# Optimization experiments

Measured on AMD Instinct MI355X. Metric: run time of the kernel, lower is better.

## Reference

```python
import jax, jax.numpy as jnp
import numpy as np

N = 100000   # nodes
E = 600000   # edges
NF = 4       # node feat dim (3 pos + 1 scalar)
EF = 5       # edge feat dim
H = 128      # hidden dim


def setup_inputs() -> dict:
    key = jax.random.key(0)
    ks = jax.random.split(key, 9)

    def lin(k, fan_in, fan_out):
        return (jax.random.normal(k, (fan_in, fan_out), dtype=jnp.float32)
                * (1.0 / np.sqrt(fan_in)))

    x = jax.random.normal(ks[0], (N, NF), dtype=jnp.float32)
    edge_index = jax.random.randint(ks[1], (2, E), 0, N, dtype=jnp.int32)
    edge_attr = jax.random.normal(ks[2], (E, EF), dtype=jnp.float32)

    return {
        "x": x,
        "edge_attr": edge_attr,
        "W1": lin(ks[3], NF, H), "b1": jnp.zeros((H,), jnp.float32),
        "W2": lin(ks[4], H, H),  "b2": jnp.zeros((H,), jnp.float32),
        "Wm1": lin(ks[5], 2 * H + EF, H), "bm1": jnp.zeros((H,), jnp.float32),
        "Wm2": lin(ks[6], H, H),          "bm2": jnp.zeros((H,), jnp.float32),
        "Wm3": lin(ks[7], H, 1),          "bm3": jnp.zeros((1,), jnp.float32),
        "edge_index": edge_index,
    }


def reference(x, edge_attr, W1, b1, W2, b2, Wm1, bm1, Wm2, bm2, Wm3, bm3,
              edge_index):
    src, dst = edge_index[0], edge_index[1]
    n = x.shape[0]

    # GCNConv: add self-loops, symmetric D^{-1/2} A D^{-1/2} normalization.
    loop = jnp.arange(n, dtype=src.dtype)
    src_sl = jnp.concatenate([src, loop])
    dst_sl = jnp.concatenate([dst, loop])
    deg = jax.ops.segment_sum(jnp.ones_like(src_sl, dtype=x.dtype),
                              dst_sl, num_segments=n)
    dinv = jnp.where(deg > 0, jax.lax.rsqrt(deg), 0.0)
    enorm = dinv[src_sl] * dinv[dst_sl]          # [E + N]

    def gcn(h, W, b):
        h = h @ W                                 # transform then propagate
        msg = h[src_sl] * enorm[:, None]          # gather + scale
        return jax.ops.segment_sum(msg, dst_sl, num_segments=n) + b

    h = jax.nn.relu(gcn(x, W1, b1))
    h = gcn(h, W2, b2)

    # Edge classifier: gather endpoints, concat with edge features, MLP.
    edge_emb = jnp.concatenate([h[src], h[dst], edge_attr], axis=1)  # [E, 2H+EF]
    z = jax.nn.relu(edge_emb @ Wm1 + bm1)
    z = jax.nn.relu(z @ Wm2 + bm2)
    out = (z @ Wm3 + bm3)[:, 0]
    return jax.nn.sigmoid(out)
```

## Files before the change

kernel.cpp:

```cpp
#include <hip/hip_runtime.h>
#include <math.h>

#define TPB 256
#define SCAN_T 256
#define SCAN_I 4
#define SCAN_CHUNK 1024

typedef __attribute__((ext_vector_type(8))) short bf16x8;
typedef __attribute__((ext_vector_type(16))) float f32x16;

static __device__ __forceinline__ short f2bf(float a) {
  unsigned ua = __builtin_bit_cast(unsigned, a);
  ua = (ua + 0x7fffu + ((ua >> 16) & 1u)) >> 16;
  return (short)ua;
}
static __device__ __forceinline__ unsigned f2bf_pack(float a, float b) {
  unsigned ua = __builtin_bit_cast(unsigned, a);
  unsigned ub = __builtin_bit_cast(unsigned, b);
  ua = (ua + 0x7fffu + ((ua >> 16) & 1u)) >> 16;
  ub = (ub + 0x7fffu + ((ub >> 16) & 1u)) >> 16;
  return ua | (ub << 16);
}
static __device__ __forceinline__ float bflo(unsigned u) {
  return __builtin_bit_cast(float, u << 16);
}
static __device__ __forceinline__ float bfhi(unsigned u) {
  return __builtin_bit_cast(float, u & 0xffff0000u);
}

__global__ void k_zero_int(int* __restrict__ p, int n) {
  int t = blockIdx.x * TPB + threadIdx.x;
  if (t < n) p[t] = 0;
}

__global__ void k_hist(const int* __restrict__ dst, int* __restrict__ deg, int E) {
  int t = blockIdx.x * TPB + threadIdx.x;
  if (t < E) atomicAdd(&deg[dst[t]], 1);
}

__global__ __launch_bounds__(SCAN_T) void k_scan_local(const int* __restrict__ deg,
                                                       int* __restrict__ loc,
                                                       int* __restrict__ bsum,
                                                       float* __restrict__ dinv, int N) {
  __shared__ int s[SCAN_T];
  int b = blockIdx.x, t = threadIdx.x;
  int base = b * SCAN_CHUNK + t * SCAN_I;
  int v[SCAN_I];
  int sum = 0;
#pragma unroll
  for (int u = 0; u < SCAN_I; u++) {
    int x = (base + u < N) ? deg[base + u] : 0;
    if (base + u < N) dinv[base + u] = rsqrtf((float)x + 1.0f);
    v[u] = sum;
    sum += x;
  }
  s[t] = sum;
  __syncthreads();
#pragma unroll
  for (int off = 1; off < SCAN_T; off <<= 1) {
    int x = (t >= off) ? s[t - off] : 0;
    __syncthreads();
    s[t] += x;
    __syncthreads();
  }
  int excl = (t == 0) ? 0 : s[t - 1];
#pragma unroll
  for (int u = 0; u < SCAN_I; u++)
    if (base + u < N) loc[base + u] = v[u] + excl;
  if (t == SCAN_T - 1) bsum[b] = s[t];
}

__global__ void k_scan_block(int* __restrict__ bsum, int nb) {
  int t = threadIdx.x;
  int i0 = 2 * t, i1 = 2 * t + 1;
  int a = (i0 < nb) ? bsum[i0] : 0;
  int b = (i1 < nb) ? bsum[i1] : 0;
  int s = a + b;
#pragma unroll
  for (int off = 1; off < 64; off <<= 1) {
    int u = __shfl_up(s, off, 64);
    if (t >= off) s += u;
  }
  int excl = s - (a + b);
  if (i0 < nb) bsum[i0] = excl;
  if (i1 < nb) bsum[i1] = excl + a;
}

__global__ void k_scan_add(int* __restrict__ rowoff, const int* __restrict__ bsum,
                           int* __restrict__ cursor, int N) {
  int t = blockIdx.x * TPB + threadIdx.x;
  if (t >= N) return;
  int ro = rowoff[t] + bsum[t / SCAN_CHUNK];
  rowoff[t] = ro;
  cursor[t] = ro;
}

__global__ void k_fill_slots(const int* __restrict__ src, const int* __restrict__ dst,
                             int* __restrict__ cursor, int* __restrict__ slots,
                             int2* __restrict__ epair, int E) {
  int e = blockIdx.x * TPB + threadIdx.x;
  if (e >= E) return;
  int d = dst[e];
  int pos = atomicAdd(&cursor[d], 1);
  slots[pos] = src[e];
  epair[pos] = make_int2(e, d);
}

__global__ void k_gcn1(const float4* __restrict__ x4, const float* __restrict__ W1,
                       const float* __restrict__ dinv, unsigned* __restrict__ tout, int N) {
  int t = blockIdx.x * TPB + threadIdx.x;
  int n = t >> 5;
  if (n >= N) return;
  int q = (t & 31) << 2;
  float4 xv = x4[n];
  float s = dinv[n];
  float r[4];
#pragma unroll
  for (int u = 0; u < 4; u++) {
    int j = q + u;
    r[u] = s * (xv.x * W1[j] + xv.y * W1[128 + j] + xv.z * W1[256 + j] + xv.w * W1[384 + j]);
  }
  uint2 p;
  p.x = f2bf_pack(r[0], r[1]);
  p.y = f2bf_pack(r[2], r[3]);
  *(uint2*)&tout[n * 64 + (q >> 1)] = p;
}

template <bool RELU>
__global__ void k_agg(const unsigned* __restrict__ ts, const int* __restrict__ rowoff,
                      const int* __restrict__ deg, const int* __restrict__ slots,
                      const float* __restrict__ dinv, const float* __restrict__ bias,
                      unsigned* __restrict__ hout, int N) {
  int t = blockIdx.x * TPB + threadIdx.x;
  int n = t >> 4;
  if (n >= N) return;
  int q = (t & 15) << 2;
  uint4 sv = *(const uint4*)&ts[(size_t)n * 64 + q];
  float a0 = bflo(sv.x), a1 = bfhi(sv.x), a2 = bflo(sv.y), a3 = bfhi(sv.y);
  float a4 = bflo(sv.z), a5 = bfhi(sv.z), a6 = bflo(sv.w), a7 = bfhi(sv.w);
  int start = rowoff[n], d = deg[n];
  for (int j0 = 0; j0 < d; j0 += 8) {
    int sl[8];
#pragma unroll
    for (int u = 0; u < 8; u++) {
      int jj = j0 + u;
      sl[u] = (jj < d) ? slots[start + jj] : -1;
    }
    uint4 v[8];
#pragma unroll
    for (int u = 0; u < 8; u++)
      v[u] = (sl[u] >= 0) ? *(const uint4*)&ts[(size_t)sl[u] * 64 + q]
                          : make_uint4(0u, 0u, 0u, 0u);
#pragma unroll
    for (int u = 0; u < 8; u++) {
      a0 += bflo(v[u].x);
      a1 += bfhi(v[u].x);
      a2 += bflo(v[u].y);
      a3 += bfhi(v[u].y);
      a4 += bflo(v[u].z);
      a5 += bfhi(v[u].z);
      a6 += bflo(v[u].w);
      a7 += bfhi(v[u].w);
    }
  }
  float sc = dinv[n];
  int col = q << 1;
  float4 b0 = *(const float4*)&bias[col];
  float4 b1 = *(const float4*)&bias[col + 4];
  a0 = a0 * sc + b0.x;
  a1 = a1 * sc + b0.y;
  a2 = a2 * sc + b0.z;
  a3 = a3 * sc + b0.w;
  a4 = a4 * sc + b1.x;
  a5 = a5 * sc + b1.y;
  a6 = a6 * sc + b1.z;
  a7 = a7 * sc + b1.w;
  if (RELU) {
    a0 = fmaxf(a0, 0.f);
    a1 = fmaxf(a1, 0.f);
    a2 = fmaxf(a2, 0.f);
    a3 = fmaxf(a3, 0.f);
    a4 = fmaxf(a4, 0.f);
    a5 = fmaxf(a5, 0.f);
    a6 = fmaxf(a6, 0.f);
    a7 = fmaxf(a7, 0.f);
  }
  uint4 p;
  p.x = f2bf_pack(a0, a1);
  p.y = f2bf_pack(a2, a3);
  p.z = f2bf_pack(a4, a5);
  p.w = f2bf_pack(a6, a7);
  *(uint4*)&hout[(size_t)n * 64 + q] = p;
}

template <bool BIAS, bool DINV>
__global__ __launch_bounds__(256, 2) void k_gemm_bf(const unsigned* __restrict__ A,
                                                    const float* __restrict__ W,
                                                    const float* __restrict__ bias,
                                                    const float* __restrict__ dinv,
                                                    unsigned* __restrict__ out, int N) {
  __shared__ unsigned sA[64 * 64];
  __shared__ float sDinv[64];
  int tid = threadIdx.x;
  int wv = tid >> 6, lane = tid & 63;
  int rg = wv >> 1, ch = wv & 1;
  int l31 = lane & 31, h = lane >> 5;

  bf16x8 wf[2][8];
  float bcol[2];
#pragma unroll
  for (int t = 0; t < 2; t++) {
    int col = ch * 64 + 2 * l31 + t;
#pragma unroll
    for (int kk = 0; kk < 8; kk++) {
      int kb = kk * 16 + h * 8;
      bf16x8 v;
#pragma unroll
      for (int u = 0; u < 8; u++) v[u] = f2bf(W[(kb + u) * 128 + col]);
      wf[t][kk] = v;
    }
    bcol[t] = BIAS ? bias[col] : 0.f;
  }

  int ntiles = (N + 63) >> 6;
  for (int tile = blockIdx.x; tile < ntiles; tile += gridDim.x) {
    __syncthreads();
    int row0 = tile << 6;
    for (int idx = tid; idx < 1024; idx += 256) {
      int r = idx >> 4, c4 = idx & 15;
      int n = row0 + r;
      uint4 v = (n < N) ? ((const uint4*)A)[(size_t)n * 16 + c4] : make_uint4(0, 0, 0, 0);
      *(uint4*)&sA[r * 64 + ((c4 * 4) ^ ((r & 15) << 2))] = v;
    }
    if (DINV && tid < 64) sDinv[tid] = (row0 + tid < N) ? dinv[row0 + tid] : 0.f;
    __syncthreads();

    int arow = rg * 32 + l31;
    const char* abase = (const char*)sA + arow * 256;
    int swz = (arow & 15) << 4;
    f32x16 acc[2];
#pragma unroll
    for (int t = 0; t < 2; t++) {
#pragma unroll
      for (int r = 0; r < 16; r++) acc[t][r] = 0.f;
    }
#pragma unroll
    for (int kk = 0; kk < 8; kk++) {
      bf16x8 a = *(const bf16x8*)(abase + ((kk * 32 + h * 16) ^ swz));
      acc[0] = __builtin_amdgcn_mfma_f32_32x32x16_bf16(a, wf[0][kk], acc[0], 0, 0, 0);
      acc[1] = __builtin_amdgcn_mfma_f32_32x32x16_bf16(a, wf[1][kk], acc[1], 0, 0, 0);
    }
#pragma unroll
    for (int r = 0; r < 16; r++) {
      int drow = (r & 3) + 8 * (r >> 2) + 4 * h;
      int n = row0 + rg * 32 + drow;
      if (n < N) {
        float v0 = acc[0][r] + bcol[0];
        float v1 = acc[1][r] + bcol[1];
        if (DINV) {
          float s = sDinv[rg * 32 + drow];
          v0 *= s;
          v1 *= s;
        }
        out[(size_t)n * 64 + ch * 32 + l31] = f2bf_pack(v0, v1);
      }
    }
  }
}

__global__ __launch_bounds__(512, 2) void k_gemm_dual(const unsigned* __restrict__ A,
                                                      const float* __restrict__ Wm1,
                                                      const float* __restrict__ bm1,
                                                      unsigned* __restrict__ out_s,
                                                      unsigned* __restrict__ out_d, int N) {
  __shared__ unsigned sA[64 * 64];
  int tid = threadIdx.x;
  int wv = tid >> 6, lane = tid & 63;
  int part = wv >> 2;
  int w4 = wv & 3;
  int rg = w4 >> 1, ch = w4 & 1;
  int l31 = lane & 31, h = lane >> 5;
  const float* W = Wm1 + (size_t)part * 128 * 128;
  unsigned* outp = part ? out_d : out_s;

  bf16x8 wf[2][8];
  float bcol[2];
#pragma unroll
  for (int t = 0; t < 2; t++) {
    int col = ch * 64 + 2 * l31 + t;
#pragma unroll
    for (int kk = 0; kk < 8; kk++) {
      int kb = kk * 16 + h * 8;
      bf16x8 v;
#pragma unroll
      for (int u = 0; u < 8; u++) v[u] = f2bf(W[(kb + u) * 128 + col]);
      wf[t][kk] = v;
    }
    bcol[t] = part ? 0.f : bm1[col];
  }

  int ntiles = (N + 63) >> 6;
  for (int tile = blockIdx.x; tile < ntiles; tile += gridDim.x) {
    __syncthreads();
    int row0 = tile << 6;
    for (int idx = tid; idx < 1024; idx += 512) {
      int r = idx >> 4, c4 = idx & 15;
      int n = row0 + r;
      uint4 v = (n < N) ? ((const uint4*)A)[(size_t)n * 16 + c4] : make_uint4(0, 0, 0, 0);
      *(uint4*)&sA[r * 64 + ((c4 * 4) ^ ((r & 15) << 2))] = v;
    }
    __syncthreads();

    int arow = rg * 32 + l31;
    const char* abase = (const char*)sA + arow * 256;
    int swz = (arow & 15) << 4;
    f32x16 acc[2];
#pragma unroll
    for (int t = 0; t < 2; t++) {
#pragma unroll
      for (int r = 0; r < 16; r++) acc[t][r] = 0.f;
    }
#pragma unroll
    for (int kk = 0; kk < 8; kk++) {
      bf16x8 a = *(const bf16x8*)(abase + ((kk * 32 + h * 16) ^ swz));
      acc[0] = __builtin_amdgcn_mfma_f32_32x32x16_bf16(a, wf[0][kk], acc[0], 0, 0, 0);
      acc[1] = __builtin_amdgcn_mfma_f32_32x32x16_bf16(a, wf[1][kk], acc[1], 0, 0, 0);
    }
#pragma unroll
    for (int r = 0; r < 16; r++) {
      int drow = (r & 3) + 8 * (r >> 2) + 4 * h;
      int n = row0 + rg * 32 + drow;
      if (n < N) {
        float v0 = acc[0][r] + bcol[0];
        float v1 = acc[1][r] + bcol[1];
        outp[(size_t)n * 64 + ch * 32 + l31] = f2bf_pack(v0, v1);
      }
    }
  }
}

__global__ __launch_bounds__(256, 3) void k_edge_mlp(
    const unsigned* __restrict__ a_s, const unsigned* __restrict__ a_d,
    const float* __restrict__ eattr, const int* __restrict__ slots,
    const int2* __restrict__ epair, const float* __restrict__ We,
    const float* __restrict__ Wm2, const float* __restrict__ bm2,
    const float* __restrict__ Wm3, const float* __restrict__ bm3,
    float* __restrict__ out, int E) {
  __shared__ unsigned sZ1[64 * 64];
  __shared__ float sEa[64][5];
  __shared__ int sSrc[64], sDst[64], sEid[64];
  __shared__ float sP[64][2];

  int tid = threadIdx.x;
  int wv = tid >> 6;
  int lane = tid & 63;
  int rg = wv >> 1;
  int ch = wv & 1;
  int l31 = lane & 31;
  int h = lane >> 5;

  bf16x8 bfr[2][8];
#pragma unroll
  for (int t = 0; t < 2; t++) {
    int col = ch * 64 + t * 32 + l31;
#pragma unroll
    for (int kk = 0; kk < 8; kk++) {
      int kb = kk * 16 + h * 8;
      bf16x8 v;
#pragma unroll
      for (int u = 0; u < 8; u++) v[u] = f2bf(Wm2[(kb + u) * 128 + col]);
      bfr[t][kk] = v;
    }
  }
  float wm3c[2], bm2c[2];
#pragma unroll
  for (int t = 0; t < 2; t++) {
    int col = ch * 64 + t * 32 + l31;
    wm3c[t] = Wm3[col];
    bm2c[t] = bm2[col];
  }
  float bm3v = bm3[0];
  float2 we[5];
#pragma unroll
  for (int j = 0; j < 5; j++) we[j] = *(const float2*)(We + j * 128 + 2 * lane);

  int ntiles = (E + 63) >> 6;
  for (int tile = blockIdx.x; tile < ntiles; tile += gridDim.x) {
    __syncthreads();
    int p0 = tile << 6;
    if (tid < 64) {
      int p = p0 + tid;
      int2 ed = (p < E) ? epair[p] : make_int2(0, 0);
      sSrc[tid] = (p < E) ? slots[p] : 0;
      sDst[tid] = ed.y;
      sEid[tid] = ed.x;
    }
    for (int idx = tid; idx < 320; idx += 256) {
      int r = idx / 5, j = idx - r * 5;
      int p = p0 + r;
      int e = (p < E) ? epair[p].x : 0;
      sEa[r][j] = (p < E) ? eattr[(size_t)e * 5 + j] : 0.f;
    }
    __syncthreads();

    unsigned ua[16], ud[16];
#pragma unroll
    for (int i = 0; i < 16; i++) {
      int r = wv * 16 + i;
      ua[i] = a_s[(size_t)sSrc[r] * 64 + lane];
      ud[i] = a_d[(size_t)sDst[r] * 64 + lane];
    }
#pragma unroll
    for (int i = 0; i < 16; i++) {
      int r = wv * 16 + i;
      float v0 = bflo(ua[i]) + bflo(ud[i]);
      float v1 = bfhi(ua[i]) + bfhi(ud[i]);
#pragma unroll
      for (int j = 0; j < 5; j++) {
        float ea = sEa[r][j];
        v0 = fmaf(ea, we[j].x, v0);
        v1 = fmaf(ea, we[j].y, v1);
      }
      v0 = fmaxf(v0, 0.f);
      v1 = fmaxf(v1, 0.f);
      sZ1[r * 64 + (lane ^ ((r & 15) << 2))] = f2bf_pack(v0, v1);
    }
    __syncthreads();

    int arow = rg * 32 + l31;
    const char* abase = (const char*)sZ1 + arow * 256;
    int swz = (arow & 15) << 4;
    float p16[16];
#pragma unroll
    for (int r = 0; r < 16; r++) p16[r] = 0.f;
#pragma unroll
    for (int t = 0; t < 2; t++) {
      f32x16 acc;
#pragma unroll
      for (int r = 0; r < 16; r++) acc[r] = 0.f;
#pragma unroll
      for (int kk = 0; kk < 8; kk++) {
        bf16x8 a = *(const bf16x8*)(abase + ((kk * 32 + h * 16) ^ swz));
        acc = __builtin_amdgcn_mfma_f32_32x32x16_bf16(a, bfr[t][kk], acc, 0, 0, 0);
      }
#pragma unroll
      for (int r = 0; r < 16; r++) {
        float z2 = fmaxf(acc[r] + bm2c[t], 0.f);
        p16[r] = fmaf(z2, wm3c[t], p16[r]);
      }
    }
#pragma unroll
    for (int r = 0; r < 16; r++) {
      float p = p16[r];
#pragma unroll
      for (int off = 16; off >= 1; off >>= 1) p += __shfl_xor(p, off, 32);
      if (l31 == 0) {
        int row = (r & 3) + 8 * (r >> 2) + 4 * h;
        sP[rg * 32 + row][ch] = p;
      }
    }
    __syncthreads();
    if (tid < 64) {
      int p = p0 + tid;
      if (p < E) {
        float pv = sP[tid][0] + sP[tid][1] + bm3v;
        out[sEid[tid]] = 1.f / (1.f + __expf(-pv));
      }
    }
  }
}

extern "C" void kernel_launch(void* const* d_in, const int* in_sizes, int n_in,
                              void* d_out, int out_size, void* d_ws, size_t ws_size,
                              hipStream_t stream) {
  const float* x = (const float*)d_in[0];
  const float* eattr = (const float*)d_in[1];
  const float* W1 = (const float*)d_in[2];
  const float* b1 = (const float*)d_in[3];
  const float* W2 = (const float*)d_in[4];
  const float* b2 = (const float*)d_in[5];
  const float* Wm1 = (const float*)d_in[6];
  const float* bm1 = (const float*)d_in[7];
  const float* Wm2 = (const float*)d_in[8];
  const float* bm2 = (const float*)d_in[9];
  const float* Wm3 = (const float*)d_in[10];
  const float* bm3 = (const float*)d_in[11];
  const int* ei = (const int*)d_in[12];
  int N = in_sizes[0] / 4;
  int E = in_sizes[12] / 2;
  const int* src = ei;
  const int* dst = ei + E;
  float* out = (float*)d_out;

  size_t npad = (size_t)((N + 63) & ~63);
  float* dinv = (float*)d_ws;
  unsigned* U1 = (unsigned*)(dinv + npad);
  unsigned* U2 = U1 + (size_t)N * 64;
  unsigned* U3 = U2 + (size_t)N * 64;
  unsigned* U4 = U3 + (size_t)N * 64;
  int* degi = (int*)(U4 + (size_t)N * 64);
  int* rowoff = degi + npad;
  int* cursor = rowoff + npad;
  int* bsum = cursor + npad;
  int* slots = bsum + 256;
  int2* epair = (int2*)(slots + ((E + 1) & ~1));

  int gN = (N + TPB - 1) / TPB;
  int gE = (E + TPB - 1) / TPB;
  int gN16 = (N * 16 + TPB - 1) / TPB;
  int gN32 = (N * 32 + TPB - 1) / TPB;
  int nb1 = (N + SCAN_CHUNK - 1) / SCAN_CHUNK;

  k_zero_int<<<gN, TPB, 0, stream>>>(degi, N);
  k_hist<<<gE, TPB, 0, stream>>>(dst, degi, E);
  k_scan_local<<<nb1, SCAN_T, 0, stream>>>(degi, rowoff, bsum, dinv, N);
  k_scan_block<<<1, 64, 0, stream>>>(bsum, nb1);
  k_scan_add<<<gN, TPB, 0, stream>>>(rowoff, bsum, cursor, N);
  k_fill_slots<<<gE, TPB, 0, stream>>>(src, dst, cursor, slots, epair, E);

  k_gcn1<<<gN32, TPB, 0, stream>>>((const float4*)x, W1, dinv, U1, N);
  k_agg<true><<<gN16, TPB, 0, stream>>>(U1, rowoff, degi, slots, dinv, b1, U2, N);

  k_gemm_bf<false, true><<<512, TPB, 0, stream>>>(U2, W2, nullptr, dinv, U1, N);
  k_agg<false><<<gN16, TPB, 0, stream>>>(U1, rowoff, degi, slots, dinv, b2, U3, N);

  k_gemm_dual<<<512, 512, 0, stream>>>(U3, Wm1, bm1, U2, U4, N);
  k_edge_mlp<<<2048, TPB, 0, stream>>>(U2, U4, eattr, slots, epair,
                                       Wm1 + 256 * 128, Wm2, bm2, Wm3, bm3, out, E);
}
```

Before: 312.6 us.

## Aggregate raw 4-dim features before applying W1 in first GCN layer

Uses linearity to reorder the first GCN layer: the scaled 4-wide input features are aggregated over neighbors first, and W1, bias and ReLU are applied after aggregation. The separate transform kernel and the 128-wide bf16 gather pass are replaced by a gather of 16-byte float4 rows. The dinv-scaled inputs are computed inside the scan kernel. This removes a full N×128 intermediate write and read and cuts per-edge gather traffic, at the cost of per-thread weight registers and a shuffle reduction per node. Aggregation now happens in fp32 before the matmul rather than on bf16-rounded transformed features, so rounding behavior shifts slightly.

```diff
diff --git a/kernel.cpp b/kernel.cpp
--- a/kernel.cpp
+++ b/kernel.cpp
@@ -41,7 +41,9 @@
 __global__ __launch_bounds__(SCAN_T) void k_scan_local(const int* __restrict__ deg,
                                                        int* __restrict__ loc,
                                                        int* __restrict__ bsum,
-                                                       float* __restrict__ dinv, int N) {
+                                                       float* __restrict__ dinv,
+                                                       const float4* __restrict__ x4,
+                                                       float4* __restrict__ xs, int N) {
   __shared__ int s[SCAN_T];
   int b = blockIdx.x, t = threadIdx.x;
   int base = b * SCAN_CHUNK + t * SCAN_I;
@@ -50,7 +52,12 @@
 #pragma unroll
   for (int u = 0; u < SCAN_I; u++) {
     int x = (base + u < N) ? deg[base + u] : 0;
-    if (base + u < N) dinv[base + u] = rsqrtf((float)x + 1.0f);
+    if (base + u < N) {
+      float dv = rsqrtf((float)x + 1.0f);
+      dinv[base + u] = dv;
+      float4 xv = x4[base + u];
+      xs[base + u] = make_float4(xv.x * dv, xv.y * dv, xv.z * dv, xv.w * dv);
+    }
     v[u] = sum;
     sum += x;
   }
@@ -106,24 +113,64 @@
   epair[pos] = make_int2(e, d);
 }
 
-__global__ void k_gcn1(const float4* __restrict__ x4, const float* __restrict__ W1,
-                       const float* __restrict__ dinv, unsigned* __restrict__ tout, int N) {
-  int t = blockIdx.x * TPB + threadIdx.x;
-  int n = t >> 5;
-  if (n >= N) return;
-  int q = (t & 31) << 2;
-  float4 xv = x4[n];
-  float s = dinv[n];
-  float r[4];
-#pragma unroll
-  for (int u = 0; u < 4; u++) {
-    int j = q + u;
-    r[u] = s * (xv.x * W1[j] + xv.y * W1[128 + j] + xv.z * W1[256 + j] + xv.w * W1[384 + j]);
-  }
-  uint2 p;
-  p.x = f2bf_pack(r[0], r[1]);
-  p.y = f2bf_pack(r[2], r[3]);
-  *(uint2*)&tout[n * 64 + (q >> 1)] = p;
+__global__ __launch_bounds__(256) void k_agg1(const float4* __restrict__ xs,
+                                              const int* __restrict__ rowoff,
+                                              const int* __restrict__ deg,
+                                              const int* __restrict__ slots,
+                                              const float* __restrict__ dinv,
+                                              const float* __restrict__ W1,
+                                              const float* __restrict__ b1,
+                                              unsigned* __restrict__ h1, int N) {
+  int u = threadIdx.x & 15;
+  float w[4][8];
+  float bb[8];
+#pragma unroll
+  for (int k = 0; k < 4; k++)
+#pragma unroll
+    for (int c = 0; c < 8; c++) w[k][c] = W1[k * 128 + u * 8 + c];
+#pragma unroll
+  for (int c = 0; c < 8; c++) bb[c] = b1[u * 8 + c];
+
+  int g0 = (blockIdx.x * TPB + threadIdx.x) >> 4;
+  int gstride = (gridDim.x * TPB) >> 4;
+  for (int n = g0; n < N; n += gstride) {
+    int start = rowoff[n], d = deg[n];
+    float4 acc = make_float4(0.f, 0.f, 0.f, 0.f);
+    for (int j = u; j < d; j += 16) {
+      float4 v = xs[slots[start + j]];
+      acc.x += v.x;
+      acc.y += v.y;
+      acc.z += v.z;
+      acc.w += v.w;
+    }
+#pragma unroll
+    for (int off = 8; off >= 1; off >>= 1) {
+      acc.x += __shfl_xor(acc.x, off, 16);
+      acc.y += __shfl_xor(acc.y, off, 16);
+      acc.z += __shfl_xor(acc.z, off, 16);
+      acc.w += __shfl_xor(acc.w, off, 16);
+    }
+    float4 xv = xs[n];
+    acc.x += xv.x;
+    acc.y += xv.y;
+    acc.z += xv.z;
+    acc.w += xv.w;
+    float sc = dinv[n];
+    uint4 o;
+    unsigned* op = (unsigned*)&o;
+#pragma unroll
+    for (int c2 = 0; c2 < 4; c2++) {
+      int c0 = 2 * c2, c1 = 2 * c2 + 1;
+      float r0 = fmaf(acc.x, w[0][c0],
+                      fmaf(acc.y, w[1][c0], fmaf(acc.z, w[2][c0], acc.w * w[3][c0])));
+      float r1 = fmaf(acc.x, w[0][c1],
+                      fmaf(acc.y, w[1][c1], fmaf(acc.z, w[2][c1], acc.w * w[3][c1])));
+      r0 = fmaxf(fmaf(r0, sc, bb[c0]), 0.f);
+      r1 = fmaxf(fmaf(r1, sc, bb[c1]), 0.f);
+      op[c2] = f2bf_pack(r0, r1);
+    }
+    *(uint4*)&h1[(size_t)n * 64 + u * 4] = o;
+  }
 }
 
 template <bool RELU>
@@ -494,7 +541,8 @@
 
   size_t npad = (size_t)((N + 63) & ~63);
   float* dinv = (float*)d_ws;
-  unsigned* U1 = (unsigned*)(dinv + npad);
+  float4* xs = (float4*)(dinv + npad);
+  unsigned* U1 = (unsigned*)(xs + npad);
   unsigned* U2 = U1 + (size_t)N * 64;
   unsigned* U3 = U2 + (size_t)N * 64;
   unsigned* U4 = U3 + (size_t)N * 64;
@@ -508,18 +556,16 @@
   int gN = (N + TPB - 1) / TPB;
   int gE = (E + TPB - 1) / TPB;
   int gN16 = (N * 16 + TPB - 1) / TPB;
-  int gN32 = (N * 32 + TPB - 1) / TPB;
   int nb1 = (N + SCAN_CHUNK - 1) / SCAN_CHUNK;
 
   k_zero_int<<<gN, TPB, 0, stream>>>(degi, N);
   k_hist<<<gE, TPB, 0, stream>>>(dst, degi, E);
-  k_scan_local<<<nb1, SCAN_T, 0, stream>>>(degi, rowoff, bsum, dinv, N);
+  k_scan_local<<<nb1, SCAN_T, 0, stream>>>(degi, rowoff, bsum, dinv, (const float4*)x, xs, N);
   k_scan_block<<<1, 64, 0, stream>>>(bsum, nb1);
   k_scan_add<<<gN, TPB, 0, stream>>>(rowoff, bsum, cursor, N);
   k_fill_slots<<<gE, TPB, 0, stream>>>(src, dst, cursor, slots, epair, E);
 
-  k_gcn1<<<gN32, TPB, 0, stream>>>((const float4*)x, W1, dinv, U1, N);
-  k_agg<true><<<gN16, TPB, 0, stream>>>(U1, rowoff, degi, slots, dinv, b1, U2, N);
+  k_agg1<<<2048, TPB, 0, stream>>>(xs, rowoff, degi, slots, dinv, W1, b1, U2, N);
 
   k_gemm_bf<false, true><<<512, TPB, 0, stream>>>(U2, W2, nullptr, dinv, U1, N);
   k_agg<false><<<gN16, TPB, 0, stream>>>(U1, rowoff, degi, slots, dinv, b2, U3, N);
```

Result: faster. 281.6 us, median of 2 (-9.9%).
